# Optimization experiments

Hardware: AMD Instinct MI355X
Metric: run time of the kernel (lower is better)

## Reference

```python
import jax, jax.numpy as jnp
import numpy as np

# --- static Cayley table for Cl(3) (8 blades) ---
def _derive_cayley_table():
    basis_gens = [(), (1,), (2,), (3,), (1, 2), (1, 3), (2, 3), (1, 2, 3)]
    gens_to_idx = {g: i for i, g in enumerate(basis_gens)}
    def reduce(a, b):
        gens = list(a) + list(b)
        sign = 1
        changed = True
        while changed:
            changed = False
            i = 0
            while i < len(gens) - 1:
                if gens[i] == gens[i + 1]:
                    gens.pop(i); gens.pop(i)
                    changed = True
                    if i > 0:
                        i -= 1
                elif gens[i] > gens[i + 1]:
                    gens[i], gens[i + 1] = gens[i + 1], gens[i]
                    sign *= -1
                    changed = True
                    i += 1
                else:
                    i += 1
        return gens_to_idx[tuple(gens)], sign
    return [[reduce(basis_gens[i], basis_gens[j]) for j in range(8)] for i in range(8)]

_TAB = _derive_cayley_table()
SI = np.array([i for i in range(8) for _ in range(8)], dtype=np.int32)
SJ = np.array([j for _ in range(8) for j in range(8)], dtype=np.int32)
TK = np.array([_TAB[i][j][0] for i in range(8) for j in range(8)], dtype=np.int32)
SG = np.array([float(_TAB[i][j][1]) for i in range(8) for j in range(8)], dtype=np.float32)

N_TOK, N_BLADE, D_BLADE, D_FFN = 8192, 8, 256, 1024
LN_EPS = 1e-5


def setup_inputs() -> dict:
    key = jax.random.key(0)
    ks = jax.random.split(key, 5)
    scale = 0.02
    return {
        'x': jax.random.normal(ks[0], (N_TOK, N_BLADE, D_BLADE), jnp.float32),
        'interaction_weights': jnp.full((64,), 0.1, jnp.float32),
        'geo_gate': jnp.asarray(0.5, jnp.float32),
        'ln_w': jnp.ones((D_BLADE,), jnp.float32),
        'ln_b': jnp.zeros((D_BLADE,), jnp.float32),
        'W_gate': jax.random.normal(ks[1], (D_BLADE, D_FFN), jnp.float32) * scale,
        'W_up': jax.random.normal(ks[2], (D_BLADE, D_FFN), jnp.float32) * scale,
        'W_down': jax.random.normal(ks[3], (D_FFN, D_BLADE), jnp.float32) * scale,
    }


def reference(x, interaction_weights, geo_gate, ln_w, ln_b, W_gate, W_up, W_down):
    si = jnp.asarray(SI); sj = jnp.asarray(SJ); tk = jnp.asarray(TK)
    sg = jnp.asarray(SG).astype(x.dtype)
    w = jax.nn.sigmoid(interaction_weights).astype(x.dtype)
    # gather blade pairs, weighted Cayley product: (N, 64, D)
    products = x[:, si, :] * x[:, sj, :] * (sg * w)[None, :, None]
    # scatter-add into target blades: (N, 8, D)
    geo = jnp.zeros_like(x).at[:, tk, :].add(products)
    g = jax.nn.sigmoid(geo_gate)
    mixed = g * geo + (1.0 - g) * x
    # LayerNorm over D
    flat = mixed.reshape(-1, x.shape[-1])
    mu = jnp.mean(flat, axis=-1, keepdims=True)
    var = jnp.var(flat, axis=-1, keepdims=True)
    flat = (flat - mu) * jax.lax.rsqrt(var + LN_EPS) * ln_w + ln_b
    # SwiGLU FFN
    h = jax.nn.silu(flat @ W_gate) * (flat @ W_up)
    out = (h @ W_down).reshape(x.shape)
    return x + out
```

## Files before the change

### kernel.cpp

```cpp
#include <hip/hip_runtime.h>
#include <hip/hip_bf16.h>
#include <hip/hip_fp8.h>

typedef __bf16 bf16x8 __attribute__((ext_vector_type(8)));
typedef float floatx4 __attribute__((ext_vector_type(4)));

constexpr int TK[64] = {
  0,1,2,3,4,5,6,7,
  1,0,4,5,2,3,7,6,
  2,4,0,6,1,7,3,5,
  3,5,6,0,7,1,2,4,
  4,2,1,7,0,6,5,3,
  5,3,7,1,6,0,4,2,
  6,7,3,2,5,4,0,1,
  7,6,5,4,3,2,1,0
};
constexpr float SGN[64] = {
  1, 1, 1, 1, 1, 1, 1, 1,
  1, 1, 1, 1, 1, 1, 1, 1,
  1,-1, 1, 1,-1,-1, 1,-1,
  1,-1,-1, 1, 1,-1,-1, 1,
  1,-1, 1, 1,-1,-1, 1,-1,
  1,-1,-1, 1, 1,-1,-1, 1,
  1, 1,-1, 1,-1, 1,-1,-1,
  1, 1,-1, 1,-1, 1,-1,-1
};

__device__ __forceinline__ void async16(const void* g, void* l) {
  __builtin_amdgcn_global_load_lds(
      (const __attribute__((address_space(1))) void*)g,
      (__attribute__((address_space(3))) void*)l, 16, 0, 0);
}

__device__ __forceinline__ unsigned char to_fp8(float v) {
  __hip_fp8_e4m3 q(v);
  return (unsigned char)q.__x;
}

__global__ __launch_bounds__(256) void transpose_cast(
    const float* __restrict__ src, __bf16* __restrict__ dst, int K, int N)
{
  __shared__ float s[32 * 33];
  const int t = threadIdx.x;
  const int k0 = blockIdx.y * 32, n0 = blockIdx.x * 32;
  const int r = t >> 5, c = t & 31;
  #pragma unroll
  for (int i = 0; i < 4; ++i)
    s[(r + i * 8) * 33 + c] = src[(size_t)(k0 + r + i * 8) * N + n0 + c];
  __syncthreads();
  #pragma unroll
  for (int i = 0; i < 4; ++i)
    dst[(size_t)(n0 + r + i * 8) * K + k0 + c] = (__bf16)s[c * 33 + r + i * 8];
}

__global__ __launch_bounds__(256) void transpose_cast_fp8(
    const float* __restrict__ src, unsigned char* __restrict__ dst, int K, int N)
{
  __shared__ float s[32 * 33];
  const int t = threadIdx.x;
  const int k0 = blockIdx.y * 32, n0 = blockIdx.x * 32;
  const int r = t >> 5, c = t & 31;
  #pragma unroll
  for (int i = 0; i < 4; ++i)
    s[(r + i * 8) * 33 + c] = src[(size_t)(k0 + r + i * 8) * N + n0 + c];
  __syncthreads();
  #pragma unroll
  for (int i = 0; i < 4; ++i)
    dst[(size_t)(n0 + r + i * 8) * K + k0 + c] = to_fp8(16.f * s[c * 33 + r + i * 8]);
}

__global__ __launch_bounds__(256) void geo_ln(
    const float* __restrict__ X,
    const float* __restrict__ IW,
    const float* __restrict__ GG,
    const float* __restrict__ LW, const float* __restrict__ LB,
    __bf16* __restrict__ F)
{
  __shared__ float sw[64];
  __shared__ float smix[8 * 256];
  __shared__ float sstat[16];
  const int t = threadIdx.x;
  const int tok = blockIdx.x;

  if (t < 64) sw[t] = SGN[t] / (1.f + __expf(-IW[t]));

  float xv[8];
  #pragma unroll
  for (int b = 0; b < 8; ++b) xv[b] = X[(size_t)tok * 2048 + b * 256 + t];
  const float g = 1.f / (1.f + __expf(-GG[0]));

  __syncthreads();

  float geo[8] = {0.f, 0.f, 0.f, 0.f, 0.f, 0.f, 0.f, 0.f};
  #pragma unroll
  for (int p = 0; p < 64; ++p)
    geo[TK[p]] += xv[p >> 3] * xv[p & 7] * sw[p];

  float mv[8];
  #pragma unroll
  for (int b = 0; b < 8; ++b) {
    mv[b] = g * geo[b] + (1.f - g) * xv[b];
    smix[b * 256 + t] = mv[b];
  }
  __syncthreads();

  const int wv = t >> 6, lane = t & 63;
  #pragma unroll
  for (int s = 0; s < 2; ++s) {
    int b = wv * 2 + s;
    float v0 = smix[b * 256 + lane];
    float v1 = smix[b * 256 + 64 + lane];
    float v2 = smix[b * 256 + 128 + lane];
    float v3 = smix[b * 256 + 192 + lane];
    float sum = v0 + v1 + v2 + v3;
    float sq  = v0*v0 + v1*v1 + v2*v2 + v3*v3;
    #pragma unroll
    for (int off = 32; off > 0; off >>= 1) {
      sum += __shfl_xor(sum, off, 64);
      sq  += __shfl_xor(sq,  off, 64);
    }
    if (lane == 0) {
      float mu  = sum * (1.f / 256.f);
      float var = sq * (1.f / 256.f) - mu * mu;
      sstat[b]     = mu;
      sstat[8 + b] = rsqrtf(var + 1e-5f);
    }
  }
  __syncthreads();

  const float lw = LW[t], lb = LB[t];
  #pragma unroll
  for (int b = 0; b < 8; ++b) {
    float v = (mv[b] - sstat[b]) * sstat[8 + b] * lw + lb;
    F[(size_t)(tok * 8 + b) * 256 + t] = (__bf16)v;
  }
}

__global__ __launch_bounds__(256, 2) void gemm_gateup(
    const __bf16* __restrict__ A,
    const __bf16* __restrict__ Bg,
    const __bf16* __restrict__ Bu,
    unsigned char* __restrict__ H)
{
  __shared__ __bf16 sA[128 * 64];
  __shared__ __bf16 sBg[128 * 64];
  __shared__ __bf16 sBu[128 * 64];
  const int t = threadIdx.x;
  const int f0 = blockIdx.x * 128;
  const int m0 = blockIdx.y * 128;
  const int lane = t & 63, wv = t >> 6;
  const int wm = wv & 1, wf = wv >> 1;
  const int l15 = lane & 15, quad = lane >> 4;

  int aoff[4], boff[4];
  #pragma unroll
  for (int i = 0; i < 4; ++i) {
    int idx = i * 256 + t, row = idx >> 3, slot = idx & 7;
    aoff[i] = (m0 + row) * 256 + (slot ^ (row & 7)) * 8;
    boff[i] = (f0 + row) * 256 + (slot ^ (row & 7)) * 8;
  }

  floatx4 zero = {0.f, 0.f, 0.f, 0.f};
  floatx4 accg[4][4], accu[4][4];
  #pragma unroll
  for (int i = 0; i < 4; ++i)
    #pragma unroll
    for (int j = 0; j < 4; ++j) { accg[i][j] = zero; accu[i][j] = zero; }

  const int xr = l15 & 7;
  for (int k = 0; k < 4; ++k) {
    const int kk = k * 64;
    #pragma unroll
    for (int i = 0; i < 4; ++i) {
      async16(A  + aoff[i] + kk, &sA[(i * 256 + t) * 8]);
      async16(Bg + boff[i] + kk, &sBg[(i * 256 + t) * 8]);
      async16(Bu + boff[i] + kk, &sBu[(i * 256 + t) * 8]);
    }
    __syncthreads();

    #pragma unroll
    for (int s = 0; s < 2; ++s) {
      const int slot = (s * 4 + quad) ^ xr;
      bf16x8 av[4], bg[4], bu[4];
      #pragma unroll
      for (int i = 0; i < 4; ++i) {
        int r = wm * 64 + i * 16 + l15;
        av[i] = *(const bf16x8*)&sA[r * 64 + slot * 8];
      }
      #pragma unroll
      for (int j = 0; j < 4; ++j) {
        int r = wf * 64 + j * 16 + l15;
        bg[j] = *(const bf16x8*)&sBg[r * 64 + slot * 8];
        bu[j] = *(const bf16x8*)&sBu[r * 64 + slot * 8];
      }
      #pragma unroll
      for (int i = 0; i < 4; ++i)
        #pragma unroll
        for (int j = 0; j < 4; ++j) {
          accg[i][j] = __builtin_amdgcn_mfma_f32_16x16x32_bf16(av[i], bg[j], accg[i][j], 0, 0, 0);
          accu[i][j] = __builtin_amdgcn_mfma_f32_16x16x32_bf16(av[i], bu[j], accu[i][j], 0, 0, 0);
        }
    }
    __syncthreads();
  }

  #pragma unroll
  for (int i = 0; i < 4; ++i)
    #pragma unroll
    for (int j = 0; j < 4; ++j)
      #pragma unroll
      for (int r = 0; r < 4; ++r) {
        int m = m0 + wm * 64 + i * 16 + quad * 4 + r;
        int f = f0 + wf * 64 + j * 16 + l15;
        float gv = accg[i][j][r];
        float uv = accu[i][j][r];
        float hv = (gv / (1.f + __expf(-gv))) * uv;
        H[(size_t)m * 1024 + f] = to_fp8(16.f * hv);
      }
}

__global__ __launch_bounds__(256, 3) void gemm_down(
    const unsigned char* __restrict__ A,
    const unsigned char* __restrict__ B,
    const float* __restrict__ X,
    float* __restrict__ O)
{
  __shared__ unsigned char sA[128 * 64];
  __shared__ unsigned char sB[256 * 64];
  const int t = threadIdx.x;
  const int m0 = blockIdx.x * 128;
  const int lane = t & 63, wv = t >> 6;
  const int wm = wv & 1, wn = wv >> 1;
  const int l15 = lane & 15, quad = lane >> 4;

  int aoff[2], boff[4];
  #pragma unroll
  for (int i = 0; i < 2; ++i) {
    int idx = i * 256 + t, row = idx >> 2, q = idx & 3;
    aoff[i] = (m0 + row) * 1024 + (q ^ ((row >> 1) & 3)) * 16;
  }
  #pragma unroll
  for (int i = 0; i < 4; ++i) {
    int idx = i * 256 + t, row = idx >> 2, q = idx & 3;
    boff[i] = row * 1024 + (q ^ ((row >> 1) & 3)) * 16;
  }

  floatx4 zero = {0.f, 0.f, 0.f, 0.f};
  floatx4 acc[4][8];
  #pragma unroll
  for (int i = 0; i < 4; ++i)
    #pragma unroll
    for (int j = 0; j < 8; ++j) acc[i][j] = zero;

  for (int k = 0; k < 16; ++k) {
    const int kk = k * 64;
    #pragma unroll
    for (int i = 0; i < 2; ++i) async16(A + aoff[i] + kk, &sA[(i * 256 + t) * 16]);
    #pragma unroll
    for (int i = 0; i < 4; ++i) async16(B + boff[i] + kk, &sB[(i * 256 + t) * 16]);
    __syncthreads();

    #pragma unroll
    for (int s = 0; s < 2; ++s) {
      const int u = s * 4 + quad;
      long av[4], bv[8];
      #pragma unroll
      for (int i = 0; i < 4; ++i) {
        int r = wm * 64 + i * 16 + l15;
        int byte = r * 64 + (((u >> 1) ^ ((r >> 1) & 3)) << 4) + (u & 1) * 8;
        av[i] = *(const long*)&sA[byte];
      }
      #pragma unroll
      for (int j = 0; j < 8; ++j) {
        int r = wn * 128 + j * 16 + l15;
        int byte = r * 64 + (((u >> 1) ^ ((r >> 1) & 3)) << 4) + (u & 1) * 8;
        bv[j] = *(const long*)&sB[byte];
      }
      #pragma unroll
      for (int i = 0; i < 4; ++i)
        #pragma unroll
        for (int j = 0; j < 8; ++j)
          acc[i][j] = __builtin_amdgcn_mfma_f32_16x16x32_fp8_fp8(av[i], bv[j], acc[i][j], 0, 0, 0);
    }
    __syncthreads();
  }

  #pragma unroll
  for (int i = 0; i < 4; ++i)
    #pragma unroll
    for (int j = 0; j < 8; ++j)
      #pragma unroll
      for (int r = 0; r < 4; ++r) {
        int m = m0 + wm * 64 + i * 16 + quad * 4 + r;
        int n = wn * 128 + j * 16 + l15;
        size_t o = (size_t)m * 256 + n;
        O[o] = X[o] + acc[i][j][r] * (1.f / 256.f);
      }
}

extern "C" void kernel_launch(void* const* d_in, const int* in_sizes, int n_in,
                              void* d_out, int out_size, void* d_ws, size_t ws_size,
                              hipStream_t stream) {
  const float* x   = (const float*)d_in[0];
  const float* iw  = (const float*)d_in[1];
  const float* gg  = (const float*)d_in[2];
  const float* lnw = (const float*)d_in[3];
  const float* lnb = (const float*)d_in[4];
  const float* Wg  = (const float*)d_in[5];
  const float* Wu  = (const float*)d_in[6];
  const float* Wd  = (const float*)d_in[7];
  float* out = (float*)d_out;

  char* ws = (char*)d_ws;
  __bf16*        flat = (__bf16*)(ws);
  unsigned char* h    = (unsigned char*)(ws + 33554432);
  __bf16*        Bg   = (__bf16*)(ws + 100663296);
  __bf16*        Bu   = (__bf16*)(ws + 101187584);
  unsigned char* Bd   = (unsigned char*)(ws + 101711872);

  transpose_cast<<<dim3(32, 8),  256, 0, stream>>>(Wg, Bg, 256, 1024);
  transpose_cast<<<dim3(32, 8),  256, 0, stream>>>(Wu, Bu, 256, 1024);
  transpose_cast_fp8<<<dim3(8, 32), 256, 0, stream>>>(Wd, Bd, 1024, 256);
  geo_ln<<<8192, 256, 0, stream>>>(x, iw, gg, lnw, lnb, flat);
  gemm_gateup<<<dim3(8, 512), 256, 0, stream>>>(flat, Bg, Bu, h);
  gemm_down<<<512, 256, 0, stream>>>(h, Bd, x, out);
}
```

Measured before the change: 318.6 us.

## Switch gate/up GEMM to 32x32 MFMA with smaller tile and LDS-staged FP8 stores

The gate/up GEMM now uses 32x32x16 bf16 MFMA instructions and a 128x64 output tile instead of 128x128, which doubles the grid and raises the occupancy target from 2 to 3 blocks per CU. The SwiGLU result is staged through shared memory so each thread writes 16-byte vectors to H rather than scattered single bytes. The down GEMM precomputes its LDS read addresses outside the k loop, and its occupancy target drops from 3 to 2 blocks per CU. The smaller tile rereads the A operand from global memory twice as often, and the extra staging step adds a barrier.

```diff
diff --git a/kernel.cpp b/kernel.cpp
--- a/kernel.cpp
+++ b/kernel.cpp
@@ -4,6 +4,7 @@
 
 typedef __bf16 bf16x8 __attribute__((ext_vector_type(8)));
 typedef float floatx4 __attribute__((ext_vector_type(4)));
+typedef float floatx16 __attribute__((ext_vector_type(16)));
 
 constexpr int TK[64] = {
   0,1,2,3,4,5,6,7,
@@ -136,90 +137,94 @@
   }
 }
 
-__global__ __launch_bounds__(256, 2) void gemm_gateup(
+__global__ __launch_bounds__(256, 3) void gemm_gateup(
     const __bf16* __restrict__ A,
     const __bf16* __restrict__ Bg,
     const __bf16* __restrict__ Bu,
     unsigned char* __restrict__ H)
 {
-  __shared__ __bf16 sA[128 * 64];
-  __shared__ __bf16 sBg[128 * 64];
-  __shared__ __bf16 sBu[128 * 64];
-  const int t = threadIdx.x;
-  const int f0 = blockIdx.x * 128;
+  __shared__ __align__(16) char smem[32768];
+  __bf16* sA  = (__bf16*)smem;
+  __bf16* sBg = (__bf16*)(smem + 16384);
+  __bf16* sBu = (__bf16*)(smem + 24576);
+  unsigned char* sH = (unsigned char*)(smem + 16384);
+
+  const int t = threadIdx.x;
+  const int f0 = blockIdx.x * 64;
   const int m0 = blockIdx.y * 128;
   const int lane = t & 63, wv = t >> 6;
   const int wm = wv & 1, wf = wv >> 1;
-  const int l15 = lane & 15, quad = lane >> 4;
-
-  int aoff[4], boff[4];
+  const int l31 = lane & 31, half = lane >> 5;
+
+  int aoff[4], boff[2];
   #pragma unroll
   for (int i = 0; i < 4; ++i) {
     int idx = i * 256 + t, row = idx >> 3, slot = idx & 7;
     aoff[i] = (m0 + row) * 256 + (slot ^ (row & 7)) * 8;
+  }
+  #pragma unroll
+  for (int i = 0; i < 2; ++i) {
+    int idx = i * 256 + t, row = idx >> 3, slot = idx & 7;
     boff[i] = (f0 + row) * 256 + (slot ^ (row & 7)) * 8;
   }
 
-  floatx4 zero = {0.f, 0.f, 0.f, 0.f};
-  floatx4 accg[4][4], accu[4][4];
-  #pragma unroll
-  for (int i = 0; i < 4; ++i)
-    #pragma unroll
-    for (int j = 0; j < 4; ++j) { accg[i][j] = zero; accu[i][j] = zero; }
-
-  const int xr = l15 & 7;
+  floatx16 accg[2], accu[2];
+  #pragma unroll
+  for (int i = 0; i < 2; ++i)
+    #pragma unroll
+    for (int r = 0; r < 16; ++r) { accg[i][r] = 0.f; accu[i][r] = 0.f; }
+
+  const int xr = l31 & 7;
+  const int rowA0 = (wm * 64 + l31) * 64;
+  const int rowA1 = rowA0 + 32 * 64;
+  const int rowB  = (wf * 32 + l31) * 64;
+
   for (int k = 0; k < 4; ++k) {
     const int kk = k * 64;
     #pragma unroll
-    for (int i = 0; i < 4; ++i) {
-      async16(A  + aoff[i] + kk, &sA[(i * 256 + t) * 8]);
+    for (int i = 0; i < 4; ++i) async16(A + aoff[i] + kk, &sA[(i * 256 + t) * 8]);
+    #pragma unroll
+    for (int i = 0; i < 2; ++i) {
       async16(Bg + boff[i] + kk, &sBg[(i * 256 + t) * 8]);
       async16(Bu + boff[i] + kk, &sBu[(i * 256 + t) * 8]);
     }
     __syncthreads();
 
     #pragma unroll
-    for (int s = 0; s < 2; ++s) {
-      const int slot = (s * 4 + quad) ^ xr;
-      bf16x8 av[4], bg[4], bu[4];
-      #pragma unroll
-      for (int i = 0; i < 4; ++i) {
-        int r = wm * 64 + i * 16 + l15;
-        av[i] = *(const bf16x8*)&sA[r * 64 + slot * 8];
-      }
-      #pragma unroll
-      for (int j = 0; j < 4; ++j) {
-        int r = wf * 64 + j * 16 + l15;
-        bg[j] = *(const bf16x8*)&sBg[r * 64 + slot * 8];
-        bu[j] = *(const bf16x8*)&sBu[r * 64 + slot * 8];
-      }
-      #pragma unroll
-      for (int i = 0; i < 4; ++i)
-        #pragma unroll
-        for (int j = 0; j < 4; ++j) {
-          accg[i][j] = __builtin_amdgcn_mfma_f32_16x16x32_bf16(av[i], bg[j], accg[i][j], 0, 0, 0);
-          accu[i][j] = __builtin_amdgcn_mfma_f32_16x16x32_bf16(av[i], bu[j], accu[i][j], 0, 0, 0);
-        }
+    for (int s = 0; s < 4; ++s) {
+      const int oct = ((s * 2 + half) ^ xr) * 8;
+      bf16x8 a0 = *(const bf16x8*)&sA[rowA0 + oct];
+      bf16x8 a1 = *(const bf16x8*)&sA[rowA1 + oct];
+      bf16x8 bg = *(const bf16x8*)&sBg[rowB + oct];
+      bf16x8 bu = *(const bf16x8*)&sBu[rowB + oct];
+      accg[0] = __builtin_amdgcn_mfma_f32_32x32x16_bf16(a0, bg, accg[0], 0, 0, 0);
+      accu[0] = __builtin_amdgcn_mfma_f32_32x32x16_bf16(a0, bu, accu[0], 0, 0, 0);
+      accg[1] = __builtin_amdgcn_mfma_f32_32x32x16_bf16(a1, bg, accg[1], 0, 0, 0);
+      accu[1] = __builtin_amdgcn_mfma_f32_32x32x16_bf16(a1, bu, accu[1], 0, 0, 0);
     }
     __syncthreads();
   }
 
   #pragma unroll
-  for (int i = 0; i < 4; ++i)
-    #pragma unroll
-    for (int j = 0; j < 4; ++j)
-      #pragma unroll
-      for (int r = 0; r < 4; ++r) {
-        int m = m0 + wm * 64 + i * 16 + quad * 4 + r;
-        int f = f0 + wf * 64 + j * 16 + l15;
-        float gv = accg[i][j][r];
-        float uv = accu[i][j][r];
-        float hv = (gv / (1.f + __expf(-gv))) * uv;
-        H[(size_t)m * 1024 + f] = to_fp8(16.f * hv);
-      }
-}
-
-__global__ __launch_bounds__(256, 3) void gemm_down(
+  for (int i = 0; i < 2; ++i)
+    #pragma unroll
+    for (int r = 0; r < 16; ++r) {
+      int crow = (r & 3) + 8 * (r >> 2) + 4 * half;
+      int m_l = wm * 64 + i * 32 + crow;
+      float gv = accg[i][r], uv = accu[i][r];
+      float hv = (gv / (1.f + __expf(-gv))) * uv;
+      sH[m_l * 64 + wf * 32 + l31] = to_fp8(16.f * hv);
+    }
+  __syncthreads();
+  #pragma unroll
+  for (int i = 0; i < 2; ++i) {
+    int chunk = i * 256 + t;
+    int m = chunk >> 2, c = chunk & 3;
+    *(int4*)&H[(size_t)(m0 + m) * 1024 + f0 + c * 16] = *(const int4*)&sH[m * 64 + c * 16];
+  }
+}
+
+__global__ __launch_bounds__(256, 2) void gemm_down(
     const unsigned char* __restrict__ A,
     const unsigned char* __restrict__ B,
     const float* __restrict__ X,
@@ -252,6 +257,22 @@
     #pragma unroll
     for (int j = 0; j < 8; ++j) acc[i][j] = zero;
 
+  int aaddr[2][4], baddr[2][8];
+  #pragma unroll
+  for (int s = 0; s < 2; ++s) {
+    const int u = s * 4 + quad;
+    #pragma unroll
+    for (int i = 0; i < 4; ++i) {
+      int r = wm * 64 + i * 16 + l15;
+      aaddr[s][i] = r * 64 + (((u >> 1) ^ ((r >> 1) & 3)) << 4) + (u & 1) * 8;
+    }
+    #pragma unroll
+    for (int j = 0; j < 8; ++j) {
+      int r = wn * 128 + j * 16 + l15;
+      baddr[s][j] = r * 64 + (((u >> 1) ^ ((r >> 1) & 3)) << 4) + (u & 1) * 8;
+    }
+  }
+
   for (int k = 0; k < 16; ++k) {
     const int kk = k * 64;
     #pragma unroll
@@ -262,20 +283,11 @@
 
     #pragma unroll
     for (int s = 0; s < 2; ++s) {
-      const int u = s * 4 + quad;
       long av[4], bv[8];
       #pragma unroll
-      for (int i = 0; i < 4; ++i) {
-        int r = wm * 64 + i * 16 + l15;
-        int byte = r * 64 + (((u >> 1) ^ ((r >> 1) & 3)) << 4) + (u & 1) * 8;
-        av[i] = *(const long*)&sA[byte];
-      }
+      for (int i = 0; i < 4; ++i) av[i] = *(const long*)&sA[aaddr[s][i]];
       #pragma unroll
-      for (int j = 0; j < 8; ++j) {
-        int r = wn * 128 + j * 16 + l15;
-        int byte = r * 64 + (((u >> 1) ^ ((r >> 1) & 3)) << 4) + (u & 1) * 8;
-        bv[j] = *(const long*)&sB[byte];
-      }
+      for (int j = 0; j < 8; ++j) bv[j] = *(const long*)&sB[baddr[s][j]];
       #pragma unroll
       for (int i = 0; i < 4; ++i)
         #pragma unroll
@@ -322,6 +334,6 @@
   transpose_cast<<<dim3(32, 8),  256, 0, stream>>>(Wu, Bu, 256, 1024);
   transpose_cast_fp8<<<dim3(8, 32), 256, 0, stream>>>(Wd, Bd, 1024, 256);
   geo_ln<<<8192, 256, 0, stream>>>(x, iw, gg, lnw, lnb, flat);
-  gemm_gateup<<<dim3(8, 512), 256, 0, stream>>>(flat, Bg, Bu, h);
+  gemm_gateup<<<dim3(16, 512), 256, 0, stream>>>(flat, Bg, Bu, h);
   gemm_down<<<512, 256, 0, stream>>>(h, Bd, x, out);
 }
```

After: 281.2 us. 11.7% less time.
